# Performance work log

Measured on AMD Instinct MI355X. Metric: run time of the kernel, lower is better.

Reference implementation:

```python
import jax, jax.numpy as jnp
import numpy as np
from jax import lax

BLOCK_LEN = 128  # ctx_len 8192 / blocks 64
NEG_INF = -1e9


def setup_inputs() -> dict:
    key = jax.random.key(0)
    ks = jax.random.split(key, 8)
    N, L, Dm = 2, 8192, 4096
    W, H, dh = 1024, 16, 64  # width = d_model*0.25
    s = lambda fan: 1.0 / np.sqrt(fan)
    return {
        "inputs": jax.random.normal(ks[0], (N, L, Dm), jnp.float32),
        "conv_w": jax.random.normal(ks[1], (3, Dm, 3 * W), jnp.float32) * s(3 * Dm),
        "conv_b": jnp.zeros((3 * W,), jnp.float32),
        "wq": jax.random.normal(ks[2], (W, H, dh), jnp.float32) * s(W),
        "bq": jnp.zeros((H, dh), jnp.float32),
        "wk": jax.random.normal(ks[3], (W, H, dh), jnp.float32) * s(W),
        "bk": jnp.zeros((H, dh), jnp.float32),
        "wv": jax.random.normal(ks[4], (W, H, dh), jnp.float32) * s(W),
        "bv": jnp.zeros((H, dh), jnp.float32),
        "wo": jax.random.normal(ks[5], (H, dh, W), jnp.float32) * s(H * dh),
        "bo": jnp.zeros((W,), jnp.float32),
        "proj_w": jax.random.normal(ks[6], (W, Dm), jnp.float32) * s(W),
        "proj_b": jnp.zeros((Dm,), jnp.float32),
    }


def reference(inputs, conv_w, conv_b, wq, bq, wk, bk, wv, bv, wo, bo, proj_w, proj_b):
    N, L, Dm = inputs.shape
    # Conv1D(kernel=3, same padding) producing q,k,v concatenated
    x = lax.conv_general_dilated(
        inputs, conv_w, window_strides=(1,), padding="SAME",
        dimension_numbers=("NWC", "WIO", "NWC")) + conv_b
    q, k, v = jnp.split(x, 3, axis=-1)  # each [N, L, W]
    W_ = q.shape[-1]
    nb = L // BLOCK_LEN
    # row attention: independent causal attention within each block
    q = q.reshape(N * nb, BLOCK_LEN, W_)
    k = k.reshape(N * nb, BLOCK_LEN, W_)
    v = v.reshape(N * nb, BLOCK_LEN, W_)
    dh = wq.shape[-1]
    qh = jnp.einsum("btd,dhe->bthe", q, wq) + bq  # [B, T, H, dh]
    kh = jnp.einsum("btd,dhe->bthe", k, wk) + bk
    vh = jnp.einsum("btd,dhe->bthe", v, wv) + bv
    scale = 1.0 / jnp.sqrt(jnp.asarray(dh, qh.dtype))
    scores = jnp.einsum("bqhe,bkhe->bhqk", qh * scale, kh)
    causal = jnp.tril(jnp.ones((BLOCK_LEN, BLOCK_LEN), bool))
    scores = jnp.where(causal, scores, NEG_INF)
    p = jax.nn.softmax(scores, axis=-1)
    o = jnp.einsum("bhqk,bkhe->bqhe", p, vh)
    o = jnp.einsum("bqhe,hed->bqd", o, wo) + bo  # MHA output projection -> width
    o = o.reshape(N, L, W_)
    return o @ proj_w + proj_b  # final Dense(d_model)
```

## Files before the change

### kernel.cpp

```cpp
#include <hip/hip_runtime.h>
#include <hip/hip_bf16.h>
#include <stdint.h>

typedef __attribute__((ext_vector_type(8))) short short8;
typedef __attribute__((ext_vector_type(4))) float f32x4;

#define AS1 __attribute__((address_space(1)))
#define AS3 __attribute__((address_space(3)))

__device__ __forceinline__ short f2bf(float x) {
    __hip_bfloat16 h = __float2bfloat16(x);
    union { __hip_bfloat16 h; short s; } u; u.h = h; return u.s;
}

__device__ __forceinline__ void gload_lds16(const short* g, short* l) {
    __builtin_amdgcn_global_load_lds((const AS1 void*)g, (AS3 void*)l, 16, 0, 0);
}

#define SBAR()   __builtin_amdgcn_s_barrier()
#define WAITV(N) asm volatile("s_waitcnt vmcnt(" #N ")")
#define SCHED0() __builtin_amdgcn_sched_barrier(0)

template<int TAPS, int MODE, bool F32OUT>
__global__ __launch_bounds__(512, 2) void gemm256(
    const short* __restrict__ A, int lda,
    const short* __restrict__ BT, int ldb, long long tapB,
    void* __restrict__ Cout, int ldc,
    const float* __restrict__ bias, int Ktiles)
{
    __shared__ __align__(16) short As[2 * 2 * 256 * 32];
    __shared__ __align__(16) short Bs[2 * 2 * 256 * 32];
    const int tid = threadIdx.x, lane = tid & 63, wid = tid >> 6;
    const int wm = wid >> 2, wn = wid & 3;
    const int m0 = blockIdx.y * 256, n0 = blockIdx.x * 256;
    const size_t arow0 = (TAPS == 3) ? ((size_t)(m0 >> 13) * 8194 + (size_t)(m0 & 8191))
                                     : (size_t)m0;
    const size_t ldaS = (size_t)lda, ldbS = (size_t)ldb, tapBS = (size_t)tapB;
    const short* Abase0 = A + arow0 * ldaS;
    const short* Bbase0 = BT + (size_t)n0 * ldbS + ((MODE == 1) ? (m0 & ~1023) : 0);
    const int c15 = lane & 15, g4 = (lane >> 4) * 4;
    const int swz = ((lane >> 4) ^ ((c15 >> 1) & 3)) * 8;
    const int srow = tid >> 2;
    const int schunk = (((tid & 3) ^ ((tid >> 3) & 3)) * 8);

#define STG_A(u, kh, buf) do { \
    const int tp_ = (TAPS == 3) ? ((u) >> 6) : 0; \
    const int kc_ = (TAPS == 3) ? (((u) & 63) << 6) : ((u) << 6); \
    const short* g_ = Abase0 + (size_t)tp_ * ldaS + kc_ + (kh) * 32 \
                      + (size_t)srow * ldaS + schunk; \
    short* l_ = As + (buf) * 16384 + (kh) * 8192 + wid * 512; \
    gload_lds16(g_, l_); \
    gload_lds16(g_ + 128 * ldaS, l_ + 4096); \
} while (0)

#define STG_B(u, kh, buf) do { \
    const int tp_ = (TAPS == 3) ? ((u) >> 6) : 0; \
    const int kc_ = (TAPS == 3) ? (((u) & 63) << 6) : ((u) << 6); \
    const short* g_ = Bbase0 + (size_t)tp_ * tapBS + kc_ + (kh) * 32 \
                      + (size_t)srow * ldbS + schunk; \
    short* l_ = Bs + (buf) * 16384 + (kh) * 8192 + wid * 512; \
    gload_lds16(g_, l_); \
    gload_lds16(g_ + 128 * ldbS, l_ + 4096); \
} while (0)

#define LDA_(buf, kk, mi) (*(const short8*)(As + (buf) * 16384 + (kk) * 8192 \
                           + (wm * 128 + (mi) * 16 + c15) * 32 + swz))
#define LDB_(buf, kk, nj) (*(const short8*)(Bs + (buf) * 16384 + (kk) * 8192 \
                           + (wn * 64 + (nj) * 16 + c15) * 32 + swz))

#define MFMA4x4(MB) do { \
    __builtin_amdgcn_s_setprio(1); \
    _Pragma("unroll") \
    for (int mi_ = 0; mi_ < 4; ++mi_) \
        _Pragma("unroll") \
        for (int nj_ = 0; nj_ < 4; ++nj_) \
            acc[(MB) + mi_][nj_] = __builtin_amdgcn_mfma_f32_16x16x32_bf16( \
                af[mi_], bf4[nj_], acc[(MB) + mi_][nj_], 0, 0, 0); \
    __builtin_amdgcn_s_setprio(0); \
} while (0)

    f32x4 acc[8][4];
    #pragma unroll
    for (int i = 0; i < 8; ++i)
        #pragma unroll
        for (int j = 0; j < 4; ++j)
            acc[i][j] = (f32x4){0.f, 0.f, 0.f, 0.f};

    STG_A(0, 0, 0); STG_B(0, 0, 0); STG_A(0, 1, 0); STG_B(0, 1, 0);
    WAITV(4); SBAR(); SCHED0();

    for (int t = 0; t < Ktiles; ++t) {
        const int c = t & 1, nb = c ^ 1;
        const bool st = (t + 1 < Ktiles);
        const int u = t + 1;
        short8 af[4], bf4[4];

        #pragma unroll
        for (int mi = 0; mi < 4; ++mi) af[mi] = LDA_(c, 0, mi);
        #pragma unroll
        for (int nj = 0; nj < 4; ++nj) bf4[nj] = LDB_(c, 0, nj);
        if (st) STG_A(u, 0, nb);
        SBAR();
        MFMA4x4(0);
        SBAR();

        #pragma unroll
        for (int mi = 0; mi < 4; ++mi) af[mi] = LDA_(c, 0, 4 + mi);
        if (st) STG_B(u, 0, nb);
        if (st) { WAITV(4); } else { WAITV(0); }
        SBAR(); SCHED0();
        MFMA4x4(4);
        SBAR();

        #pragma unroll
        for (int mi = 0; mi < 4; ++mi) af[mi] = LDA_(c, 1, mi);
        #pragma unroll
        for (int nj = 0; nj < 4; ++nj) bf4[nj] = LDB_(c, 1, nj);
        if (st) STG_A(u, 1, nb);
        SBAR();
        MFMA4x4(0);
        SBAR();

        #pragma unroll
        for (int mi = 0; mi < 4; ++mi) af[mi] = LDA_(c, 1, 4 + mi);
        if (st) STG_B(u, 1, nb);
        if (st) { WAITV(4); } else { WAITV(0); }
        SBAR(); SCHED0();
        MFMA4x4(4);
        SBAR();
    }

    float bv[4];
    #pragma unroll
    for (int nj = 0; nj < 4; ++nj)
        bv[nj] = bias ? bias[n0 + wn * 64 + nj * 16 + c15] : 0.f;
    #pragma unroll
    for (int mi = 0; mi < 8; ++mi) {
        #pragma unroll
        for (int r = 0; r < 4; ++r) {
            const size_t row = (size_t)m0 + wm * 128 + mi * 16 + g4 + r;
            #pragma unroll
            for (int nj = 0; nj < 4; ++nj) {
                const int col = n0 + wn * 64 + nj * 16 + c15;
                const float v = acc[mi][nj][r] + bv[nj];
                if (F32OUT) ((float*)Cout)[row * (size_t)ldc + col] = v;
                else        ((short*)Cout)[row * (size_t)ldc + col] = f2bf(v);
            }
        }
    }
#undef STG_A
#undef STG_B
#undef LDA_
#undef LDB_
#undef MFMA4x4
}

__global__ __launch_bounds__(256) void attn_kernel(
    const short* __restrict__ qkvh, short* __restrict__ obuf)
{
    __shared__ __align__(16) char smem[54272];
    short* qs = (short*)smem;
    short* ks = (short*)smem + 9216;
    short* vt = (short*)(smem + 36864);
    short* ps = (short*)smem;
    short* os = (short*)smem;

    const int tid = threadIdx.x, lane = tid & 63, wid = tid >> 6;
    const int h = blockIdx.x, b = blockIdx.y;
    const size_t base = (size_t)b * 128 * 3072 + (size_t)h * 64;

    for (int i = tid; i < 1024; i += 256) {
        const int row = i >> 3, c8 = i & 7;
        const size_t g = base + (size_t)row * 3072 + c8 * 8;
        *(short8*)(qs + row * 72 + c8 * 8) = *(const short8*)(qkvh + g);
        *(short8*)(ks + row * 72 + c8 * 8) = *(const short8*)(qkvh + g + 1024);
        short8 vv = *(const short8*)(qkvh + g + 2048);
        #pragma unroll
        for (int j = 0; j < 8; ++j) vt[(c8 * 8 + j) * 136 + row] = vv[j];
    }
    __syncthreads();

    const int c15 = lane & 15, g8 = (lane >> 4) * 8, g4 = (lane >> 4) * 4;
    const int r0 = wid * 32;

    f32x4 sacc[2][8];
    #pragma unroll
    for (int mi = 0; mi < 2; ++mi)
        #pragma unroll
        for (int nj = 0; nj < 8; ++nj)
            sacc[mi][nj] = (f32x4){0.f, 0.f, 0.f, 0.f};
    #pragma unroll
    for (int kk = 0; kk < 2; ++kk) {
        short8 aq[2];
        #pragma unroll
        for (int mi = 0; mi < 2; ++mi)
            aq[mi] = *(const short8*)(qs + (r0 + mi * 16 + c15) * 72 + kk * 32 + g8);
        #pragma unroll
        for (int nj = 0; nj < 8; ++nj) {
            short8 bk8 = *(const short8*)(ks + (nj * 16 + c15) * 72 + kk * 32 + g8);
            #pragma unroll
            for (int mi = 0; mi < 2; ++mi)
                sacc[mi][nj] = __builtin_amdgcn_mfma_f32_16x16x32_bf16(
                    aq[mi], bk8, sacc[mi][nj], 0, 0, 0);
        }
    }
    __syncthreads();

    #pragma unroll
    for (int mi = 0; mi < 2; ++mi) {
        #pragma unroll
        for (int r = 0; r < 4; ++r) {
            const int qrow = r0 + mi * 16 + g4 + r;
            float m = -3.0e38f, pv[8];
            #pragma unroll
            for (int nj = 0; nj < 8; ++nj) {
                float s = sacc[mi][nj][r] * 0.125f;
                if (nj * 16 + c15 > qrow) s = -1.0e9f;
                pv[nj] = s; m = fmaxf(m, s);
            }
            #pragma unroll
            for (int off = 8; off >= 1; off >>= 1) m = fmaxf(m, __shfl_xor(m, off));
            float sum = 0.f;
            #pragma unroll
            for (int nj = 0; nj < 8; ++nj) { float p = __expf(pv[nj] - m); pv[nj] = p; sum += p; }
            #pragma unroll
            for (int off = 8; off >= 1; off >>= 1) sum += __shfl_xor(sum, off);
            const float inv = 1.0f / sum;
            #pragma unroll
            for (int nj = 0; nj < 8; ++nj)
                ps[qrow * 136 + nj * 16 + c15] = f2bf(pv[nj] * inv);
        }
    }
    __syncthreads();

    f32x4 oacc[2][4];
    #pragma unroll
    for (int mi = 0; mi < 2; ++mi)
        #pragma unroll
        for (int nj = 0; nj < 4; ++nj)
            oacc[mi][nj] = (f32x4){0.f, 0.f, 0.f, 0.f};
    #pragma unroll
    for (int kt = 0; kt < 4; ++kt) {
        short8 ap[2];
        #pragma unroll
        for (int mi = 0; mi < 2; ++mi)
            ap[mi] = *(const short8*)(ps + (r0 + mi * 16 + c15) * 136 + kt * 32 + g8);
        #pragma unroll
        for (int nj = 0; nj < 4; ++nj) {
            short8 bv8 = *(const short8*)(vt + (nj * 16 + c15) * 136 + kt * 32 + g8);
            #pragma unroll
            for (int mi = 0; mi < 2; ++mi)
                oacc[mi][nj] = __builtin_amdgcn_mfma_f32_16x16x32_bf16(
                    ap[mi], bv8, oacc[mi][nj], 0, 0, 0);
        }
    }
    __syncthreads();

    #pragma unroll
    for (int mi = 0; mi < 2; ++mi)
        #pragma unroll
        for (int r = 0; r < 4; ++r)
            #pragma unroll
            for (int nj = 0; nj < 4; ++nj)
                os[(r0 + mi * 16 + g4 + r) * 72 + nj * 16 + c15] = f2bf(oacc[mi][nj][r]);
    __syncthreads();

    for (int i = tid; i < 1024; i += 256) {
        const int row = i >> 3, c8 = i & 7;
        *(short8*)(obuf + (size_t)b * 128 * 1024 + (size_t)h * 64
                   + (size_t)row * 1024 + c8 * 8) =
            *(const short8*)(os + row * 72 + c8 * 8);
    }
}

__global__ void pad_convert_inputs(const float* __restrict__ in, short* __restrict__ out)
{
    const int row = blockIdx.x;
    const int n = row / 8194, l = row % 8194;
    short* orow = out + (size_t)row * 4096;
    if (l == 0 || l == 8193) {
        for (int i = threadIdx.x; i < 512; i += 256) {
            uint4 z; z.x = z.y = z.z = z.w = 0u;
            *(uint4*)(orow + i * 8) = z;
        }
    } else {
        const float* irow = in + ((size_t)n * 8192 + (l - 1)) * 4096;
        for (int i = threadIdx.x; i < 512; i += 256) {
            float4 a = *(const float4*)(irow + i * 8);
            float4 b = *(const float4*)(irow + i * 8 + 4);
            short8 v;
            v[0] = f2bf(a.x); v[1] = f2bf(a.y); v[2] = f2bf(a.z); v[3] = f2bf(a.w);
            v[4] = f2bf(b.x); v[5] = f2bf(b.y); v[6] = f2bf(b.z); v[7] = f2bf(b.w);
            *(short8*)(orow + i * 8) = v;
        }
    }
}

__global__ void transpose_convert(const float* __restrict__ in, short* __restrict__ out,
                                  int R, int C)
{
    __shared__ float tile[32][33];
    const int tx = threadIdx.x & 31, ty = threadIdx.x >> 5;
    const int bx = blockIdx.x * 32, by = blockIdx.y * 32;
    #pragma unroll
    for (int i = 0; i < 32; i += 8)
        tile[ty + i][tx] = in[(size_t)(by + ty + i) * C + bx + tx];
    __syncthreads();
    #pragma unroll
    for (int i = 0; i < 32; i += 8)
        out[(size_t)(bx + ty + i) * R + by + tx] = f2bf(tile[tx][ty + i]);
}

__global__ void convert_bf16(const float* __restrict__ in, short* __restrict__ out, int n8)
{
    const int idx = blockIdx.x * 256 + threadIdx.x;
    if (idx < n8) {
        float4 a = *(const float4*)(in + (size_t)idx * 8);
        float4 b = *(const float4*)(in + (size_t)idx * 8 + 4);
        short8 v;
        v[0] = f2bf(a.x); v[1] = f2bf(a.y); v[2] = f2bf(a.z); v[3] = f2bf(a.w);
        v[4] = f2bf(b.x); v[5] = f2bf(b.y); v[6] = f2bf(b.z); v[7] = f2bf(b.w);
        *(short8*)(out + (size_t)idx * 8) = v;
    }
}

__global__ void fuse_bias(const float* __restrict__ bo, const float* __restrict__ projw,
                          const float* __restrict__ projb, float* __restrict__ outb)
{
    const int j = blockIdx.x * 256 + threadIdx.x;
    float s = projb[j];
    for (int w = 0; w < 1024; ++w) s = fmaf(bo[w], projw[(size_t)w * 4096 + j], s);
    outb[j] = s;
}

__global__ void fuse_bias_qkv(const float* __restrict__ conv_b,
                              const float* __restrict__ wq, const float* __restrict__ bq,
                              const float* __restrict__ wk, const float* __restrict__ bk,
                              const float* __restrict__ wv, const float* __restrict__ bv,
                              float* __restrict__ outb)
{
    const int o = blockIdx.x * 256 + threadIdx.x;
    const int p = o >> 10, e = o & 1023;
    const float* w = (p == 0) ? wq : (p == 1) ? wk : wv;
    const float* bb = (p == 0) ? bq : (p == 1) ? bk : bv;
    const float* cb = conv_b + p * 1024;
    float s = bb[e];
    for (int d = 0; d < 1024; ++d) s = fmaf(cb[d], w[(size_t)d * 1024 + e], s);
    outb[o] = s;
}

extern "C" void kernel_launch(void* const* d_in, const int* in_sizes, int n_in,
                              void* d_out, int out_size, void* d_ws, size_t ws_size,
                              hipStream_t stream)
{
    const float* inputs = (const float*)d_in[0];
    const float* conv_w = (const float*)d_in[1];
    const float* conv_b = (const float*)d_in[2];
    const float* wq     = (const float*)d_in[3];
    const float* bq     = (const float*)d_in[4];
    const float* wk     = (const float*)d_in[5];
    const float* bk     = (const float*)d_in[6];
    const float* wv     = (const float*)d_in[7];
    const float* bv     = (const float*)d_in[8];
    const float* wo     = (const float*)d_in[9];
    const float* bo     = (const float*)d_in[10];
    const float* proj_w = (const float*)d_in[11];
    const float* proj_b = (const float*)d_in[12];

    char* ws = (char*)d_ws;
    short* in_pad = (short*)(ws + 0);
    short* cw_bf  = (short*)(ws + 134283264);
    short* qkvh   = (short*)(ws + 134283264);
    short* W2T    = (short*)(ws + 234946560);
    short* wq_t   = (short*)(ws + 310444032);
    short* wo_bf  = (short*)(ws + 316735488);
    short* proj_t = (short*)(ws + 318832640);
    short* WfT    = (short*)(ws + 327221248);
    float* bfused = (float*)(ws + 335609856);
    float* b2     = (float*)(ws + 335626240);
    short* o_buf  = (short*)(ws + 0);

    dim3 blk(256), blk5(512);

    pad_convert_inputs<<<16388, blk, 0, stream>>>(inputs, in_pad);
    convert_bf16<<<18432, blk, 0, stream>>>(conv_w, cw_bf, 4718592);
    transpose_convert<<<dim3(32, 32), blk, 0, stream>>>(wq, wq_t, 1024, 1024);
    transpose_convert<<<dim3(32, 32), blk, 0, stream>>>(wk, wq_t + 1048576, 1024, 1024);
    transpose_convert<<<dim3(32, 32), blk, 0, stream>>>(wv, wq_t + 2097152, 1024, 1024);
    transpose_convert<<<dim3(128, 32), blk, 0, stream>>>(proj_w, proj_t, 1024, 4096);
    convert_bf16<<<512, blk, 0, stream>>>(wo, wo_bf, 131072);
    fuse_bias<<<16, blk, 0, stream>>>(bo, proj_w, proj_b, bfused);
    fuse_bias_qkv<<<12, blk, 0, stream>>>(conv_b, wq, bq, wk, bk, wv, bv, b2);

    gemm256<1, 0, false><<<dim3(4, 16), blk5, 0, stream>>>(
        proj_t, 1024, wo_bf, 1024, 0, WfT, 1024, nullptr, 16);
    for (int t = 0; t < 3; ++t)
        gemm256<1, 1, false><<<dim3(16, 12), blk5, 0, stream>>>(
            wq_t, 1024, cw_bf + (size_t)t * 4096 * 3072, 3072, 0,
            W2T + (size_t)t * 3072 * 4096, 4096, nullptr, 16);
    gemm256<3, 0, false><<<dim3(12, 64), blk5, 0, stream>>>(
        in_pad, 4096, W2T, 4096, (long long)3072 * 4096, qkvh, 3072, b2, 192);

    attn_kernel<<<dim3(16, 128), blk, 0, stream>>>(qkvh, o_buf);

    gemm256<1, 0, true><<<dim3(16, 64), blk5, 0, stream>>>(
        o_buf, 1024, WfT, 1024, 0, d_out, 4096, bfused, 16);
}
```

Before: 1.665 ms.

## Load GEMM B operand straight from global into registers, bypassing LDS

Removes the LDS staging buffer for the B matrix in the 256x256 GEMM. Each wave now loads its own B fragments straight from global memory into registers, double-buffered across K half-steps, while A is still staged through LDS. This halves LDS footprint and drops several barriers per K-tile. In exchange the B reads are strided per lane and repeated by the two wave rows that share the same columns, which adds global/L2 traffic, and the hand-tuned vmcnt waits now depend on how the compiler mixes in the register loads.

```diff
diff --git a/kernel.cpp b/kernel.cpp
--- a/kernel.cpp
+++ b/kernel.cpp
@@ -29,7 +29,6 @@
     const float* __restrict__ bias, int Ktiles)
 {
     __shared__ __align__(16) short As[2 * 2 * 256 * 32];
-    __shared__ __align__(16) short Bs[2 * 2 * 256 * 32];
     const int tid = threadIdx.x, lane = tid & 63, wid = tid >> 6;
     const int wm = wid >> 2, wn = wid & 3;
     const int m0 = blockIdx.y * 256, n0 = blockIdx.x * 256;
@@ -38,7 +37,7 @@
     const size_t ldaS = (size_t)lda, ldbS = (size_t)ldb, tapBS = (size_t)tapB;
     const short* Abase0 = A + arow0 * ldaS;
     const short* Bbase0 = BT + (size_t)n0 * ldbS + ((MODE == 1) ? (m0 & ~1023) : 0);
-    const int c15 = lane & 15, g4 = (lane >> 4) * 4;
+    const int c15 = lane & 15, g4 = (lane >> 4) * 4, g8 = (lane >> 4) * 8;
     const int swz = ((lane >> 4) ^ ((c15 >> 1) & 3)) * 8;
     const int srow = tid >> 2;
     const int schunk = (((tid & 3) ^ ((tid >> 3) & 3)) * 8);
@@ -53,29 +52,23 @@
     gload_lds16(g_ + 128 * ldaS, l_ + 4096); \
 } while (0)
 
-#define STG_B(u, kh, buf) do { \
-    const int tp_ = (TAPS == 3) ? ((u) >> 6) : 0; \
-    const int kc_ = (TAPS == 3) ? (((u) & 63) << 6) : ((u) << 6); \
-    const short* g_ = Bbase0 + (size_t)tp_ * tapBS + kc_ + (kh) * 32 \
-                      + (size_t)srow * ldbS + schunk; \
-    short* l_ = Bs + (buf) * 16384 + (kh) * 8192 + wid * 512; \
-    gload_lds16(g_, l_); \
-    gload_lds16(g_ + 128 * ldbS, l_ + 4096); \
-} while (0)
-
 #define LDA_(buf, kk, mi) (*(const short8*)(As + (buf) * 16384 + (kk) * 8192 \
                            + (wm * 128 + (mi) * 16 + c15) * 32 + swz))
-#define LDB_(buf, kk, nj) (*(const short8*)(Bs + (buf) * 16384 + (kk) * 8192 \
-                           + (wn * 64 + (nj) * 16 + c15) * 32 + swz))
-
-#define MFMA4x4(MB) do { \
+
+#define BG(tt, kk, nj) (*(const short8*)(Bbase0 \
+    + (size_t)((TAPS == 3) ? ((tt) >> 6) : 0) * tapBS \
+    + (size_t)(wn * 64 + (nj) * 16 + c15) * ldbS \
+    + ((TAPS == 3) ? (((tt) & 63) << 6) : ((tt) << 6)) + (kk) * 32 + g8))
+
+#define MFMA4x4B(MB, B0, B1, B2, B3) do { \
     __builtin_amdgcn_s_setprio(1); \
     _Pragma("unroll") \
-    for (int mi_ = 0; mi_ < 4; ++mi_) \
-        _Pragma("unroll") \
-        for (int nj_ = 0; nj_ < 4; ++nj_) \
-            acc[(MB) + mi_][nj_] = __builtin_amdgcn_mfma_f32_16x16x32_bf16( \
-                af[mi_], bf4[nj_], acc[(MB) + mi_][nj_], 0, 0, 0); \
+    for (int mi_ = 0; mi_ < 4; ++mi_) { \
+        acc[(MB) + mi_][0] = __builtin_amdgcn_mfma_f32_16x16x32_bf16(af[mi_], B0, acc[(MB) + mi_][0], 0, 0, 0); \
+        acc[(MB) + mi_][1] = __builtin_amdgcn_mfma_f32_16x16x32_bf16(af[mi_], B1, acc[(MB) + mi_][1], 0, 0, 0); \
+        acc[(MB) + mi_][2] = __builtin_amdgcn_mfma_f32_16x16x32_bf16(af[mi_], B2, acc[(MB) + mi_][2], 0, 0, 0); \
+        acc[(MB) + mi_][3] = __builtin_amdgcn_mfma_f32_16x16x32_bf16(af[mi_], B3, acc[(MB) + mi_][3], 0, 0, 0); \
+    } \
     __builtin_amdgcn_s_setprio(0); \
 } while (0)
 
@@ -86,48 +79,38 @@
         for (int j = 0; j < 4; ++j)
             acc[i][j] = (f32x4){0.f, 0.f, 0.f, 0.f};
 
-    STG_A(0, 0, 0); STG_B(0, 0, 0); STG_A(0, 1, 0); STG_B(0, 1, 0);
-    WAITV(4); SBAR(); SCHED0();
+    short8 af[4];
+    short8 bC0, bC1, bC2, bC3;
+    short8 bN0, bN1, bN2, bN3;
+
+    STG_A(0, 0, 0); STG_A(0, 1, 0);
+    bC0 = BG(0, 0, 0); bC1 = BG(0, 0, 1); bC2 = BG(0, 0, 2); bC3 = BG(0, 0, 3);
+    WAITV(0); SBAR(); SCHED0();
 
     for (int t = 0; t < Ktiles; ++t) {
         const int c = t & 1, nb = c ^ 1;
         const bool st = (t + 1 < Ktiles);
         const int u = t + 1;
-        short8 af[4], bf4[4];
-
+
+        WAITV(6); SBAR(); SCHED0();
         #pragma unroll
         for (int mi = 0; mi < 4; ++mi) af[mi] = LDA_(c, 0, mi);
-        #pragma unroll
-        for (int nj = 0; nj < 4; ++nj) bf4[nj] = LDB_(c, 0, nj);
+        bN0 = BG(t, 1, 0); bN1 = BG(t, 1, 1); bN2 = BG(t, 1, 2); bN3 = BG(t, 1, 3);
         if (st) STG_A(u, 0, nb);
-        SBAR();
-        MFMA4x4(0);
-        SBAR();
-
+        MFMA4x4B(0, bC0, bC1, bC2, bC3);
         #pragma unroll
         for (int mi = 0; mi < 4; ++mi) af[mi] = LDA_(c, 0, 4 + mi);
-        if (st) STG_B(u, 0, nb);
-        if (st) { WAITV(4); } else { WAITV(0); }
-        SBAR(); SCHED0();
-        MFMA4x4(4);
-        SBAR();
-
+        MFMA4x4B(4, bC0, bC1, bC2, bC3);
+
+        WAITV(6); SBAR(); SCHED0();
         #pragma unroll
         for (int mi = 0; mi < 4; ++mi) af[mi] = LDA_(c, 1, mi);
-        #pragma unroll
-        for (int nj = 0; nj < 4; ++nj) bf4[nj] = LDB_(c, 1, nj);
         if (st) STG_A(u, 1, nb);
-        SBAR();
-        MFMA4x4(0);
-        SBAR();
-
+        if (st) { bC0 = BG(u, 0, 0); bC1 = BG(u, 0, 1); bC2 = BG(u, 0, 2); bC3 = BG(u, 0, 3); }
+        MFMA4x4B(0, bN0, bN1, bN2, bN3);
         #pragma unroll
         for (int mi = 0; mi < 4; ++mi) af[mi] = LDA_(c, 1, 4 + mi);
-        if (st) STG_B(u, 1, nb);
-        if (st) { WAITV(4); } else { WAITV(0); }
-        SBAR(); SCHED0();
-        MFMA4x4(4);
-        SBAR();
+        MFMA4x4B(4, bN0, bN1, bN2, bN3);
     }
 
     float bv[4];
@@ -149,10 +132,9 @@
         }
     }
 #undef STG_A
-#undef STG_B
 #undef LDA_
-#undef LDB_
-#undef MFMA4x4
+#undef BG
+#undef MFMA4x4B
 }
 
 __global__ __launch_bounds__(256) void attn_kernel(
```

Result: slower. 2.249 ms (+35.0%).

## Add dedicated conv3 GEMM that reuses one A tile across all three taps

Applied to the files above, without the earlier changes.

Replaces the generic three-tap GEMM with a dedicated kernel. Each K step stages a 272-row A tile once and reads it at row offsets 0, 1 and 2 for the three taps, instead of reloading a shifted A tile from global memory for every tap. The B tiles for all three taps are staged together, using a per-offset XOR swizzle. This cuts A-side global traffic roughly threefold, but raises LDS use, uses a simpler full-drain barrier per step, and may pressure registers.

```diff
diff --git a/kernel.cpp b/kernel.cpp
--- a/kernel.cpp
+++ b/kernel.cpp
@@ -20,11 +20,111 @@
 #define SBAR()   __builtin_amdgcn_s_barrier()
 #define WAITV(N) asm volatile("s_waitcnt vmcnt(" #N ")")
 #define SCHED0() __builtin_amdgcn_sched_barrier(0)
-
-template<int TAPS, int MODE, bool F32OUT>
+#define VMCNT0_BAR() do { WAITV(0); SBAR(); SCHED0(); } while (0)
+
+__global__ __launch_bounds__(512, 2) void conv3_gemm(
+    const short* __restrict__ A,
+    const short* __restrict__ BT,
+    short* __restrict__ Cout,
+    const float* __restrict__ bias)
+{
+    __shared__ __align__(16) short As[2 * 272 * 32];
+    __shared__ __align__(16) short Bs[2 * 3 * 256 * 32];
+    const int tid = threadIdx.x, lane = tid & 63, wid = tid >> 6;
+    const int wm = wid >> 2, wn = wid & 3;
+    const int m0 = blockIdx.y * 256, n0 = blockIdx.x * 256;
+    const size_t arow0 = (size_t)(m0 >> 13) * 8194 + (size_t)(m0 & 8191);
+    const short* Abase = A + arow0 * 4096;
+    const short* Bbase = BT + (size_t)n0 * 4096;
+    const int c15 = lane & 15, g = lane >> 4, g4 = g * 4;
+    const int xr0 = (c15 >> 1) & 3;
+    const int xr1 = ((c15 + 1) >> 1) & 3;
+    const int xr2 = ((c15 + 2) >> 1) & 3;
+    const int srow = tid >> 2;
+    const int schunk = (((tid & 3) ^ ((tid >> 3) & 3)) * 8);
+    const int srowX = lane >> 2;
+    const int schunkX = (((lane & 3) ^ ((lane >> 3) & 3)) * 8);
+
+#define STAGE(s, buf) do { \
+    const int kc_ = (s) * 32; \
+    const short* ga_ = Abase + (size_t)srow * 4096 + kc_ + schunk; \
+    short* la_ = As + (buf) * 8704 + wid * 512; \
+    gload_lds16(ga_, la_); \
+    gload_lds16(ga_ + 128 * 4096, la_ + 4096); \
+    if (wid == 7) \
+        gload_lds16(Abase + (size_t)(256 + srowX) * 4096 + kc_ + schunkX, \
+                    As + (buf) * 8704 + 256 * 32); \
+    _Pragma("unroll") \
+    for (int tp_ = 0; tp_ < 3; ++tp_) { \
+        const short* gb_ = Bbase + (size_t)tp_ * 3072 * 4096 \
+                           + (size_t)srow * 4096 + kc_ + schunk; \
+        short* lb_ = Bs + (buf) * 24576 + tp_ * 8192 + wid * 512; \
+        gload_lds16(gb_, lb_); \
+        gload_lds16(gb_ + 128 * 4096, lb_ + 4096); \
+    } \
+} while (0)
+
+#define LDA_T(buf, mi, T, XR) (*(const short8*)(As + (buf) * 8704 \
+    + (wm * 128 + (mi) * 16 + c15 + (T)) * 32 + ((g ^ (XR)) * 8)))
+#define LDB_T(buf, tp, nj) (*(const short8*)(Bs + (buf) * 24576 + (tp) * 8192 \
+    + (wn * 64 + (nj) * 16 + c15) * 32 + ((g ^ xr0) * 8)))
+
+    f32x4 acc[8][4];
+    #pragma unroll
+    for (int i = 0; i < 8; ++i)
+        #pragma unroll
+        for (int j = 0; j < 4; ++j)
+            acc[i][j] = (f32x4){0.f, 0.f, 0.f, 0.f};
+
+    STAGE(0, 0);
+
+    for (int s = 0; s < 128; ++s) {
+        const int c = s & 1;
+        VMCNT0_BAR();
+        if (s + 1 < 128) STAGE(s + 1, c ^ 1);
+        #pragma unroll
+        for (int tp = 0; tp < 3; ++tp) {
+            const int xr = (tp == 0) ? xr0 : (tp == 1) ? xr1 : xr2;
+            short8 b0 = LDB_T(c, tp, 0), b1 = LDB_T(c, tp, 1);
+            short8 b2f = LDB_T(c, tp, 2), b3 = LDB_T(c, tp, 3);
+            __builtin_amdgcn_s_setprio(1);
+            #pragma unroll
+            for (int mi = 0; mi < 8; ++mi) {
+                short8 a = LDA_T(c, mi, tp, xr);
+                acc[mi][0] = __builtin_amdgcn_mfma_f32_16x16x32_bf16(a, b0, acc[mi][0], 0, 0, 0);
+                acc[mi][1] = __builtin_amdgcn_mfma_f32_16x16x32_bf16(a, b1, acc[mi][1], 0, 0, 0);
+                acc[mi][2] = __builtin_amdgcn_mfma_f32_16x16x32_bf16(a, b2f, acc[mi][2], 0, 0, 0);
+                acc[mi][3] = __builtin_amdgcn_mfma_f32_16x16x32_bf16(a, b3, acc[mi][3], 0, 0, 0);
+            }
+            __builtin_amdgcn_s_setprio(0);
+        }
+    }
+
+    float bv[4];
+    #pragma unroll
+    for (int nj = 0; nj < 4; ++nj)
+        bv[nj] = bias[n0 + wn * 64 + nj * 16 + c15];
+    #pragma unroll
+    for (int mi = 0; mi < 8; ++mi) {
+        #pragma unroll
+        for (int r = 0; r < 4; ++r) {
+            const size_t row = (size_t)m0 + wm * 128 + mi * 16 + g4 + r;
+            #pragma unroll
+            for (int nj = 0; nj < 4; ++nj) {
+                const int col = n0 + wn * 64 + nj * 16 + c15;
+                Cout[row * 3072 + col] = f2bf(acc[mi][nj][r] + bv[nj]);
+            }
+        }
+    }
+#undef STAGE
+#undef LDA_T
+#undef LDB_T
+}
+
+template<int MODE, bool F32OUT>
 __global__ __launch_bounds__(512, 2) void gemm256(
     const short* __restrict__ A, int lda,
-    const short* __restrict__ BT, int ldb, long long tapB,
+    const short* __restrict__ BT, int ldb,
     void* __restrict__ Cout, int ldc,
     const float* __restrict__ bias, int Ktiles)
 {
@@ -33,10 +133,8 @@
     const int tid = threadIdx.x, lane = tid & 63, wid = tid >> 6;
     const int wm = wid >> 2, wn = wid & 3;
     const int m0 = blockIdx.y * 256, n0 = blockIdx.x * 256;
-    const size_t arow0 = (TAPS == 3) ? ((size_t)(m0 >> 13) * 8194 + (size_t)(m0 & 8191))
-                                     : (size_t)m0;
-    const size_t ldaS = (size_t)lda, ldbS = (size_t)ldb, tapBS = (size_t)tapB;
-    const short* Abase0 = A + arow0 * ldaS;
+    const size_t ldaS = (size_t)lda, ldbS = (size_t)ldb;
+    const short* Abase0 = A + (size_t)m0 * ldaS;
     const short* Bbase0 = BT + (size_t)n0 * ldbS + ((MODE == 1) ? (m0 & ~1023) : 0);
     const int c15 = lane & 15, g4 = (lane >> 4) * 4;
     const int swz = ((lane >> 4) ^ ((c15 >> 1) & 3)) * 8;
@@ -44,20 +142,14 @@
     const int schunk = (((tid & 3) ^ ((tid >> 3) & 3)) * 8);
 
 #define STG_A(u, kh, buf) do { \
-    const int tp_ = (TAPS == 3) ? ((u) >> 6) : 0; \
-    const int kc_ = (TAPS == 3) ? (((u) & 63) << 6) : ((u) << 6); \
-    const short* g_ = Abase0 + (size_t)tp_ * ldaS + kc_ + (kh) * 32 \
-                      + (size_t)srow * ldaS + schunk; \
+    const short* g_ = Abase0 + ((u) << 6) + (kh) * 32 + (size_t)srow * ldaS + schunk; \
     short* l_ = As + (buf) * 16384 + (kh) * 8192 + wid * 512; \
     gload_lds16(g_, l_); \
     gload_lds16(g_ + 128 * ldaS, l_ + 4096); \
 } while (0)
 
 #define STG_B(u, kh, buf) do { \
-    const int tp_ = (TAPS == 3) ? ((u) >> 6) : 0; \
-    const int kc_ = (TAPS == 3) ? (((u) & 63) << 6) : ((u) << 6); \
-    const short* g_ = Bbase0 + (size_t)tp_ * tapBS + kc_ + (kh) * 32 \
-                      + (size_t)srow * ldbS + schunk; \
+    const short* g_ = Bbase0 + ((u) << 6) + (kh) * 32 + (size_t)srow * ldbS + schunk; \
     short* l_ = Bs + (buf) * 16384 + (kh) * 8192 + wid * 512; \
     gload_lds16(g_, l_); \
     gload_lds16(g_ + 128 * ldbS, l_ + 4096); \
@@ -392,17 +484,16 @@
     fuse_bias<<<16, blk, 0, stream>>>(bo, proj_w, proj_b, bfused);
     fuse_bias_qkv<<<12, blk, 0, stream>>>(conv_b, wq, bq, wk, bk, wv, bv, b2);
 
-    gemm256<1, 0, false><<<dim3(4, 16), blk5, 0, stream>>>(
-        proj_t, 1024, wo_bf, 1024, 0, WfT, 1024, nullptr, 16);
+    gemm256<0, false><<<dim3(4, 16), blk5, 0, stream>>>(
+        proj_t, 1024, wo_bf, 1024, WfT, 1024, nullptr, 16);
     for (int t = 0; t < 3; ++t)
-        gemm256<1, 1, false><<<dim3(16, 12), blk5, 0, stream>>>(
-            wq_t, 1024, cw_bf + (size_t)t * 4096 * 3072, 3072, 0,
+        gemm256<1, false><<<dim3(16, 12), blk5, 0, stream>>>(
+            wq_t, 1024, cw_bf + (size_t)t * 4096 * 3072, 3072,
             W2T + (size_t)t * 3072 * 4096, 4096, nullptr, 16);
-    gemm256<3, 0, false><<<dim3(12, 64), blk5, 0, stream>>>(
-        in_pad, 4096, W2T, 4096, (long long)3072 * 4096, qkvh, 3072, b2, 192);
+    conv3_gemm<<<dim3(12, 64), blk5, 0, stream>>>(in_pad, W2T, qkvh, b2);
 
     attn_kernel<<<dim3(16, 128), blk, 0, stream>>>(qkvh, o_buf);
 
-    gemm256<1, 0, true><<<dim3(16, 64), blk5, 0, stream>>>(
-        o_buf, 1024, WfT, 1024, 0, d_out, 4096, bfused, 16);
-}
+    gemm256<0, true><<<dim3(16, 64), blk5, 0, stream>>>(
+        o_buf, 1024, WfT, 1024, d_out, 4096, bfused, 16);
+}
```

After: 1.598 ms. -4.1%, faster.
